# Performance work log

Measured on AMD Instinct MI355X. Metric: run time of the kernel, lower is better.

## Reference

```python
import jax, jax.numpy as jnp
import numpy as np

B, D, H, DH, NQ, NK = 64, 768, 8, 128, 256, 256


def _ln(x, g, b, eps=1e-5):
    m = x.mean(-1, keepdims=True)
    v = ((x - m) ** 2).mean(-1, keepdims=True)
    return (x - m) / jnp.sqrt(v + eps) * g + b


def setup_inputs() -> dict:
    key = jax.random.key(0)
    ks = jax.random.split(key, 16)
    w = lambda k, s: jax.random.normal(k, s, jnp.float32) * 0.02
    return {
        'emb_cause': jax.random.normal(ks[0], (B, D), jnp.float32),
        'emb_action': jax.random.normal(ks[1], (B, D), jnp.float32),
        'tok_cause': jax.random.normal(ks[2], (B, NK, D), jnp.float32),
        'tok_effect': jax.random.normal(ks[3], (B, NQ, D), jnp.float32),
        'fuse_ln_g': jnp.ones(2 * D), 'fuse_ln_b': jnp.zeros(2 * D),
        'fuse_w1': w(ks[4], (2 * D, D)), 'fuse_b1': jnp.zeros(D),
        'fuse_w2': w(ks[5], (D, D)), 'fuse_b2': jnp.zeros(D),
        'delta_ln_g': jnp.ones(D), 'delta_ln_b': jnp.zeros(D),
        'delta_w': w(ks[6], (D, D)), 'delta_b': jnp.zeros(D),
        'qg_w': w(ks[7], (D, H * DH)), 'qg_b': jnp.zeros(H * DH),
        'kg_w': w(ks[8], (D, H * DH)), 'kg_b': jnp.zeros(H * DH),
        'eff_ln_g': jnp.ones(D), 'eff_ln_b': jnp.zeros(D),
        'eff_w1': w(ks[9], (D, D)), 'eff_b1': jnp.zeros(D),
        'eff_w2': w(ks[10], (D, D)), 'eff_b2': jnp.zeros(D),
        'u_w': w(ks[11], (D, H * DH)),
        'v_w': w(ks[12], (D, H * DH)),
        'logit_scale': jnp.zeros(()),
    }


def reference(emb_cause, emb_action, tok_cause, tok_effect,
              fuse_ln_g, fuse_ln_b, fuse_w1, fuse_b1, fuse_w2, fuse_b2,
              delta_ln_g, delta_ln_b, delta_w, delta_b,
              qg_w, qg_b, kg_w, kg_b,
              eff_ln_g, eff_ln_b, eff_w1, eff_b1, eff_w2, eff_b2,
              u_w, v_w, logit_scale):
    # fuse: LN -> Linear -> GELU(exact) -> Linear (dropout = identity, eval)
    ctx_in = jnp.concatenate([emb_cause, emb_action], axis=-1)  # (B, 2D)
    h = jax.nn.gelu(_ln(ctx_in, fuse_ln_g, fuse_ln_b) @ fuse_w1 + fuse_b1, approximate=False)
    ctx = h @ fuse_w2 + fuse_b2  # (B, D)

    delta_e = _ln(ctx, delta_ln_g, delta_ln_b) @ delta_w + delta_b  # (B, D)
    pooled_effect = tok_effect.mean(axis=1)  # (B, D)
    e_shifted = pooled_effect + delta_e

    eh = jax.nn.gelu(_ln(ctx, eff_ln_g, eff_ln_b) @ eff_w1 + eff_b1, approximate=False)
    effect_pred = eh @ eff_w2 + eff_b2  # (B, D)

    q_gate = 1.0 + jnp.tanh(jax.nn.silu(ctx @ qg_w + qg_b)).reshape(B, H, DH)
    k_gate = 1.0 + jnp.tanh(jax.nn.silu(ctx @ kg_w + kg_b)).reshape(B, H, DH)

    # logit bias: torch code materializes (B,H,Nq,Nk,Dh); equivalent math is a
    # per-head inner product u.v (independent of q) broadcast over Nq.
    u = (e_shifted @ u_w).reshape(B, H, DH)            # (B, H, Dh)
    v = (tok_cause @ v_w).reshape(B, NK, H, DH)        # (B, Nk, H, Dh)
    bias = jnp.einsum('bhd,bkhd->bhk', u, v) / np.float32(np.sqrt(DH))
    logit_bias = jnp.exp(logit_scale) * jnp.broadcast_to(bias[:, :, None, :], (B, H, NQ, NK))

    return (q_gate, k_gate, e_shifted, delta_e, logit_bias, effect_pred)
```

## Files before the change

### kernel.cpp

```cpp
#include <hip/hip_runtime.h>
#include <math.h>

#define TPB 256

typedef float vf4 __attribute__((ext_vector_type(4)));

__device__ __forceinline__ float gelu_f(float x) {
    return 0.5f * x * (1.0f + erff(x * 0.70710678118654752f));
}
__device__ __forceinline__ float gate_f(float x) {
    float si = x / (1.0f + expf(-x));
    return 1.0f + tanhf(si);
}

template <class XL>
__device__ __forceinline__ void gemm_tile(XL xload, const float* __restrict__ W, int Wld, int cb,
                                          int k0, int kslice, float* part, int totN, int gcol, int s,
                                          float* __restrict__ xs, float* __restrict__ wt)
{
    const int t = threadIdx.x;
    const int tr4 = (t >> 4) << 2;
    const int tc4 = (t & 15) << 2;
    const int a  = t >> 5, kk = t & 31;
    const int wk = t >> 6, wc = t & 63;
    float xv[8], wv[8];
#pragma unroll
    for (int j = 0; j < 8; ++j) {
        xv[j] = xload(a + 8 * j, k0 + kk);
        wv[j] = W[(size_t)(k0 + wk + 4 * j) * Wld + cb + wc];
    }
    float acc[4][4] = {{0.f,0.f,0.f,0.f},{0.f,0.f,0.f,0.f},{0.f,0.f,0.f,0.f},{0.f,0.f,0.f,0.f}};
    for (int kc = 0; kc < kslice; kc += 32) {
#pragma unroll
        for (int j = 0; j < 8; ++j) {
            xs[kk * 68 + a + 8 * j] = xv[j];
            wt[(wk + 4 * j) * 68 + wc] = wv[j];
        }
        __syncthreads();
        int kn = kc + 32;
        if (kn < kslice) {
#pragma unroll
            for (int j = 0; j < 8; ++j) {
                xv[j] = xload(a + 8 * j, k0 + kn + kk);
                wv[j] = W[(size_t)(k0 + kn + wk + 4 * j) * Wld + cb + wc];
            }
        }
#pragma unroll
        for (int k = 0; k < 32; ++k) {
            float4 xq = *(const float4*)&xs[k * 68 + tr4];
            float4 wq = *(const float4*)&wt[k * 68 + tc4];
            acc[0][0] += xq.x * wq.x; acc[0][1] += xq.x * wq.y; acc[0][2] += xq.x * wq.z; acc[0][3] += xq.x * wq.w;
            acc[1][0] += xq.y * wq.x; acc[1][1] += xq.y * wq.y; acc[1][2] += xq.y * wq.z; acc[1][3] += xq.y * wq.w;
            acc[2][0] += xq.z * wq.x; acc[2][1] += xq.z * wq.y; acc[2][2] += xq.z * wq.z; acc[2][3] += xq.z * wq.w;
            acc[3][0] += xq.w * wq.x; acc[3][1] += xq.w * wq.y; acc[3][2] += xq.w * wq.z; acc[3][3] += xq.w * wq.w;
        }
        __syncthreads();
    }
    float* pp = part + (size_t)(s * 64 + tr4) * totN + gcol + tc4;
#pragma unroll
    for (int i = 0; i < 4; ++i)
#pragma unroll
        for (int j = 0; j < 4; ++j)
            pp[i * totN + j] = acc[i][j];
}

#define GEMM_LDS __shared__ float xs[32 * 68]; __shared__ float wt[32 * 68];

__device__ __forceinline__ void pool_task(const float* __restrict__ tok_effect,
                                          float* __restrict__ pp, int m, int t)
{
    int cch = m % 3, b = (m / 3) % 64, qz = m / 192;
    int c = cch * TPB + t;
    const float* base = tok_effect + (size_t)(b * 256 + qz * 64) * 768 + c;
    float s = 0.f;
#pragma unroll 16
    for (int q = 0; q < 64; ++q) s += __builtin_nontemporal_load(base + (size_t)q * 768);
    pp[(qz * 64 + b) * 768 + c] = s;
}

struct G1Args {
    const float *ec, *ea, *flg, *flb, *w1;
    const float *dg, *db, *eg, *eb, *delta_w, *eff_w1;
    const float *tok_effect;
    float *part1, *pp, *stats1, *gW1, *bW1, *dgW, *dbW, *egW, *ebW;
};
__global__ __launch_bounds__(256) void k_g1(G1Args A)
{
    GEMM_LDS;
    __shared__ float red[8];
    const int t = threadIdx.x;
    if (blockIdx.x < 144) {
        int ct = blockIdx.x % 12, s = blockIdx.x / 12;
        auto xl = [&](int r, int k) {
            float raw = (k < 768) ? A.ec[r * 768 + k] : A.ea[r * 768 + (k - 768)];
            return raw * A.flg[k];
        };
        gemm_tile(xl, A.w1, 768, ct * 64, s * 128, 128, A.part1, 768, ct * 64, s, xs, wt);
    } else if (blockIdx.x < 528) {
        pool_task(A.tok_effect, A.pp, blockIdx.x - 144, t);
    } else if (blockIdx.x < 592) {
        int r = blockIdx.x - 528;
        float sum = 0.f, sq = 0.f;
#pragma unroll
        for (int j = 0; j < 6; ++j) {
            int c = t + j * TPB;
            float x = (c < 768) ? A.ec[r * 768 + c] : A.ea[r * 768 + (c - 768)];
            sum += x; sq += x * x;
        }
#pragma unroll
        for (int o_ = 32; o_ > 0; o_ >>= 1) { sum += __shfl_xor(sum, o_); sq += __shfl_xor(sq, o_); }
        if ((t & 63) == 0) { red[t >> 6] = sum; red[4 + (t >> 6)] = sq; }
        __syncthreads();
        if (t == 0) {
            float s = red[0] + red[1] + red[2] + red[3];
            float q = red[4] + red[5] + red[6] + red[7];
            float mean = s * (1.f / 1536.f);
            A.stats1[2 * r]     = mean;
            A.stats1[2 * r + 1] = rsqrtf(q * (1.f / 1536.f) - mean * mean + 1e-5f);
        }
    } else {
        int m = blockIdx.x - 592;
        int id = m / 12, chunk = m % 12;
        const float* vec; const float* W; int K; float* out;
        switch (id) {
            case 0: vec = A.flg; W = A.w1;      K = 1536; out = A.gW1; break;
            case 1: vec = A.flb; W = A.w1;      K = 1536; out = A.bW1; break;
            case 2: vec = A.dg;  W = A.delta_w; K = 768;  out = A.dgW; break;
            case 3: vec = A.db;  W = A.delta_w; K = 768;  out = A.dbW; break;
            case 4: vec = A.eg;  W = A.eff_w1;  K = 768;  out = A.egW; break;
            default: vec = A.eb; W = A.eff_w1;  K = 768;  out = A.ebW; break;
        }
        int col = chunk * 64 + (t & 63);
        int stripe = t >> 6;
        float acc = 0.f;
#pragma unroll 16
        for (int c = stripe; c < K; c += 4)
            acc += vec[c] * W[(size_t)c * 768 + col];
        xs[stripe * 64 + (t & 63)] = acc;
        __syncthreads();
        if (t < 64)
            out[chunk * 64 + t] = xs[t] + xs[64 + t] + xs[128 + t] + xs[192 + t];
    }
}

struct G2Args {
    const float *part1, *b1, *w2, *stats1, *gW1, *bW1;
    const float *tok_effect;
    float *part2, *pp;
};
__global__ __launch_bounds__(256) void k_g2(G2Args A)
{
    GEMM_LDS;
    if (blockIdx.x >= 144) {
        pool_task(A.tok_effect, A.pp, blockIdx.x - 144 + 384, threadIdx.x);
        return;
    }
    int ct = blockIdx.x % 12, s = blockIdx.x / 12;
    auto xl = [&](int r, int k) {
        float v = 0.f;
#pragma unroll
        for (int q = 0; q < 12; ++q) v += A.part1[(size_t)(q * 64 + r) * 768 + k];
        float m = A.stats1[2 * r], rs = A.stats1[2 * r + 1];
        return gelu_f(rs * (v - m * A.gW1[k]) + A.bW1[k] + A.b1[k]);
    };
    gemm_tile(xl, A.w2, 768, ct * 64, s * 64, 64, A.part2, 768, ct * 64, s, xs, wt);
}

struct GAArgs {
    const float *part2, *b2, *dg, *eg;
    const float *delta_w, *eff_w1, *qg_w, *kg_w;
    float *partA, *stats2;
};
__global__ __launch_bounds__(256) void k_gA(GAArgs A)
{
    GEMM_LDS;
    __shared__ float red[8];
    const int t = threadIdx.x;
    if (blockIdx.x >= 448) {
        int r = blockIdx.x - 448;
        float sum = 0.f, sq = 0.f;
#pragma unroll
        for (int j = 0; j < 3; ++j) {
            int c = t + j * TPB;
            float x = A.b2[c];
#pragma unroll
            for (int q = 0; q < 12; ++q) x += A.part2[(size_t)(q * 64 + r) * 768 + c];
            sum += x; sq += x * x;
        }
#pragma unroll
        for (int o_ = 32; o_ > 0; o_ >>= 1) { sum += __shfl_xor(sum, o_); sq += __shfl_xor(sq, o_); }
        if ((t & 63) == 0) { red[t >> 6] = sum; red[4 + (t >> 6)] = sq; }
        __syncthreads();
        if (t == 0) {
            float s = red[0] + red[1] + red[2] + red[3];
            float q = red[4] + red[5] + red[6] + red[7];
            float mean = s * (1.f / 768.f);
            A.stats2[2 * r]     = mean;
            A.stats2[2 * r + 1] = rsqrtf(q * (1.f / 768.f) - mean * mean + 1e-5f);
        }
        return;
    }
    int ct = blockIdx.x % 56, s = blockIdx.x / 56;
    auto ctxv = [&](int r, int k) {
        float v = A.b2[k];
#pragma unroll
        for (int q = 0; q < 12; ++q) v += A.part2[(size_t)(q * 64 + r) * 768 + k];
        return v;
    };
    if (ct < 12) {
        auto xl = [&](int r, int k) { return ctxv(r, k) * A.dg[k]; };
        gemm_tile(xl, A.delta_w, 768, ct * 64, s * 96, 96, A.partA, 3584, ct * 64, s, xs, wt);
    } else if (ct < 24) {
        auto xl = [&](int r, int k) { return ctxv(r, k) * A.eg[k]; };
        gemm_tile(xl, A.eff_w1, 768, (ct - 12) * 64, s * 96, 96, A.partA, 3584, ct * 64, s, xs, wt);
    } else {
        auto xl = [&](int r, int k) { return ctxv(r, k); };
        const float* W = (ct < 40) ? A.qg_w : A.kg_w;
        int cb = (ct < 40) ? (ct - 24) * 64 : (ct - 40) * 64;
        gemm_tile(xl, W, 1024, cb, s * 96, 96, A.partA, 3584, ct * 64, s, xs, wt);
    }
}

struct MidArgs {
    const float *partA, *pp, *stats2, *dgW, *dbW, *egW, *ebW;
    const float *delta_b, *eff_b1, *qg_b, *kg_b, *eff_w2, *u_w;
    float *partB, *out_de, *out_es, *out_qg, *out_kg;
};
__global__ __launch_bounds__(256) void k_mid(MidArgs A)
{
    GEMM_LDS;
    const int t = threadIdx.x;
    if (blockIdx.x < 28) {
#pragma unroll
        for (int ii = 0; ii < 32; ++ii) {
            int idx = blockIdx.x * TPB + t + ii * 7168;
            int r = idx / 3584, c = idx - r * 3584;
            if (c >= 768 && c < 1536) continue;
            float v = 0.f;
#pragma unroll
            for (int q = 0; q < 8; ++q) v += A.partA[(size_t)(q * 64 + r) * 3584 + c];
            if (c < 768) {
                float m = A.stats2[2 * r], rs = A.stats2[2 * r + 1];
                float de = rs * (v - m * A.dgW[c]) + A.dbW[c] + A.delta_b[c];
                A.out_de[r * 768 + c] = de;
                float s4 = A.pp[r * 768 + c] + A.pp[(64 + r) * 768 + c]
                         + A.pp[(128 + r) * 768 + c] + A.pp[(192 + r) * 768 + c];
                A.out_es[r * 768 + c] = de + s4 * (1.f / 256.f);
            } else if (c < 2560) {
                A.out_qg[r * 1024 + (c - 1536)] = gate_f(v + A.qg_b[c - 1536]);
            } else {
                A.out_kg[r * 1024 + (c - 2560)] = gate_f(v + A.kg_b[c - 2560]);
            }
        }
    } else {
        int m = blockIdx.x - 28;
        int ct = m % 28, s = m / 28;
        if (ct < 12) {
            auto xl = [&](int r, int k) {
                float v = 0.f;
#pragma unroll
                for (int q = 0; q < 8; ++q) v += A.partA[(size_t)(q * 64 + r) * 3584 + 768 + k];
                float mm = A.stats2[2 * r], rs = A.stats2[2 * r + 1];
                return gelu_f(rs * (v - mm * A.egW[k]) + A.ebW[k] + A.eff_b1[k]);
            };
            gemm_tile(xl, A.eff_w2, 768, ct * 64, s * 96, 96, A.partB, 1792, ct * 64, s, xs, wt);
        } else {
            auto xl = [&](int r, int k) {
                float v = 0.f;
#pragma unroll
                for (int q = 0; q < 8; ++q) v += A.partA[(size_t)(q * 64 + r) * 3584 + k];
                float mm = A.stats2[2 * r], rs = A.stats2[2 * r + 1];
                float de = rs * (v - mm * A.dgW[k]) + A.dbW[k] + A.delta_b[k];
                float s4 = A.pp[r * 768 + k] + A.pp[(64 + r) * 768 + k]
                         + A.pp[(128 + r) * 768 + k] + A.pp[(192 + r) * 768 + k];
                return de + s4 * (1.f / 256.f);
            };
            gemm_tile(xl, A.u_w, 1024, (ct - 12) * 64, s * 96, 96, A.partB, 1792, ct * 64, s, xs, wt);
        }
    }
}

__global__ __launch_bounds__(256) void k_tail(const float* __restrict__ partB, const float* __restrict__ eff_b2,
                                              const float* __restrict__ v_w,
                                              float* __restrict__ out_ep, float* __restrict__ wu)
{
    const int t = threadIdx.x;
    if (blockIdx.x < 6) {
#pragma unroll
        for (int ii = 0; ii < 32; ++ii) {
            int idx = blockIdx.x * TPB + t + ii * 1536;
            int r = idx / 768, c = idx - r * 768;
            float v = eff_b2[c];
#pragma unroll
            for (int q = 0; q < 8; ++q) v += partB[(size_t)(q * 64 + r) * 1792 + c];
            out_ep[r * 768 + c] = v;
        }
    } else {
        __shared__ float us[64 * 132];
        int m = blockIdx.x - 6;
        int h = m / 12, ctile = m % 12;
        for (int n = t; n < 8192; n += TPB) {
            int b = n >> 7, d = n & 127;
            float v = 0.f;
#pragma unroll
            for (int q = 0; q < 8; ++q) v += partB[(size_t)(q * 64 + b) * 1792 + 768 + h * 128 + d];
            us[b * 132 + d] = v;
        }
        __syncthreads();
        int c = ctile * 64 + (t >> 2);
        int bo = t & 3;
        const float* vr = v_w + (size_t)c * 1024 + h * 128;
        float acc[16];
#pragma unroll
        for (int i = 0; i < 16; ++i) acc[i] = 0.f;
        for (int d = 0; d < 128; d += 4) {
            float4 w4 = *(const float4*)(vr + d);
#pragma unroll
            for (int i = 0; i < 16; ++i) {
                const float* ub = &us[(4 * i + bo) * 132 + d];
                acc[i] += w4.x * ub[0] + w4.y * ub[1] + w4.z * ub[2] + w4.w * ub[3];
            }
        }
#pragma unroll
        for (int i = 0; i < 16; ++i) {
            int b = 4 * i + bo;
            wu[(b * 8 + h) * 768 + c] = acc[i];
        }
    }
}

__global__ __launch_bounds__(512) void k_biasbc(const float* __restrict__ tok_cause, const float* __restrict__ wu,
                         const float* __restrict__ ls_ptr, float* __restrict__ out_lb)
{
    int b = blockIdx.x, kt = blockIdx.y;
    __shared__ float wuh[8 * 768];
    __shared__ float bsm[8 * 32];
    for (int n = threadIdx.x; n < 6144; n += 512)
        wuh[n] = wu[b * 6144 + n];
    __syncthreads();
    const int lane = threadIdx.x & 63, w = threadIdx.x >> 6;
    vf4 wur[3][8];
#pragma unroll
    for (int j = 0; j < 3; ++j)
#pragma unroll
        for (int h = 0; h < 8; ++h)
            wur[j][h] = *(const vf4*)&wuh[h * 768 + (lane + 64 * j) * 4];
    float scale = expf(ls_ptr[0]) * 0.08838834764831845f;
#pragma unroll
    for (int rr = 0; rr < 4; ++rr) {
        int rl = w * 4 + rr;
        int row = kt * 32 + rl;
        const vf4* tr = (const vf4*)(tok_cause + ((size_t)b * 256 + row) * 768);
        vf4 t0 = tr[lane];
        vf4 t1 = tr[lane + 64];
        vf4 t2 = tr[lane + 128];
        float acc[8];
#pragma unroll
        for (int h = 0; h < 8; ++h) {
            acc[h] = t0.x * wur[0][h].x + t0.y * wur[0][h].y + t0.z * wur[0][h].z + t0.w * wur[0][h].w
                   + t1.x * wur[1][h].x + t1.y * wur[1][h].y + t1.z * wur[1][h].z + t1.w * wur[1][h].w
                   + t2.x * wur[2][h].x + t2.y * wur[2][h].y + t2.z * wur[2][h].z + t2.w * wur[2][h].w;
        }
#pragma unroll
        for (int h = 0; h < 8; ++h) {
            float vv = acc[h];
#pragma unroll
            for (int o_ = 32; o_ > 0; o_ >>= 1) vv += __shfl_xor(vv, o_);
            if (lane == 0) bsm[h * 32 + rl] = vv * scale;
        }
    }
    __syncthreads();
    const vf4* bs4 = (const vf4*)bsm;
    vf4* o4 = (vf4*)out_lb;
    int v = threadIdx.x & 7, sq0 = threadIdx.x >> 3;
#pragma unroll
    for (int it = 0; it < 32; ++it) {
        int seg = sq0 + it * 64;
        int h = seg >> 8, q = seg & 255;
        vf4 val = bs4[h * 8 + v];
        __builtin_nontemporal_store(val, &o4[(((size_t)(b * 8 + h) * 256 + q) << 6) + kt * 8 + v]);
    }
}

extern "C" void kernel_launch(void* const* d_in, const int* in_sizes, int n_in,
                              void* d_out, int out_size, void* d_ws, size_t ws_size,
                              hipStream_t stream)
{
    (void)in_sizes; (void)n_in; (void)out_size; (void)ws_size;
    const float* emb_cause  = (const float*)d_in[0];
    const float* emb_action = (const float*)d_in[1];
    const float* tok_cause  = (const float*)d_in[2];
    const float* tok_effect = (const float*)d_in[3];
    const float* fuse_ln_g  = (const float*)d_in[4];
    const float* fuse_ln_b  = (const float*)d_in[5];
    const float* fuse_w1    = (const float*)d_in[6];
    const float* fuse_b1    = (const float*)d_in[7];
    const float* fuse_w2    = (const float*)d_in[8];
    const float* fuse_b2    = (const float*)d_in[9];
    const float* delta_ln_g = (const float*)d_in[10];
    const float* delta_ln_b = (const float*)d_in[11];
    const float* delta_w    = (const float*)d_in[12];
    const float* delta_b    = (const float*)d_in[13];
    const float* qg_w       = (const float*)d_in[14];
    const float* qg_b       = (const float*)d_in[15];
    const float* kg_w       = (const float*)d_in[16];
    const float* kg_b       = (const float*)d_in[17];
    const float* eff_ln_g   = (const float*)d_in[18];
    const float* eff_ln_b   = (const float*)d_in[19];
    const float* eff_w1     = (const float*)d_in[20];
    const float* eff_b1     = (const float*)d_in[21];
    const float* eff_w2     = (const float*)d_in[22];
    const float* eff_b2     = (const float*)d_in[23];
    const float* u_w        = (const float*)d_in[24];
    const float* v_w        = (const float*)d_in[25];
    const float* logit_sc   = (const float*)d_in[26];

    float* ws = (float*)d_ws;
    float* pp     = ws + 0;
    float* wu     = ws + 196608;
    float* stats1 = ws + 589824;
    float* stats2 = ws + 589952;
    float* gW1    = ws + 590080;
    float* bW1    = ws + 590848;
    float* dgW    = ws + 591616;
    float* dbW    = ws + 592384;
    float* egW    = ws + 593152;
    float* ebW    = ws + 593920;

    float* out    = (float*)d_out;
    float* out_qg = out + 0;
    float* out_kg = out + 65536;
    float* out_es = out + 131072;
    float* out_de = out + 180224;
    float* out_lb = out + 229376;
    float* out_ep = out + 33783808;

    float* pbase = out_lb + 20000000;
    float* part1 = pbase;
    float* part2 = pbase + 589824;
    float* partA = pbase + 1179648;
    float* partB = pbase + 3014656;

    {
        G1Args A; A.ec = emb_cause; A.ea = emb_action;
        A.flg = fuse_ln_g; A.flb = fuse_ln_b; A.w1 = fuse_w1;
        A.dg = delta_ln_g; A.db = delta_ln_b; A.eg = eff_ln_g; A.eb = eff_ln_b;
        A.delta_w = delta_w; A.eff_w1 = eff_w1;
        A.tok_effect = tok_effect;
        A.part1 = part1; A.pp = pp; A.stats1 = stats1;
        A.gW1 = gW1; A.bW1 = bW1; A.dgW = dgW; A.dbW = dbW; A.egW = egW; A.ebW = ebW;
        k_g1<<<664, TPB, 0, stream>>>(A);
    }
    {
        G2Args A; A.part1 = part1; A.b1 = fuse_b1; A.w2 = fuse_w2;
        A.stats1 = stats1; A.gW1 = gW1; A.bW1 = bW1;
        A.tok_effect = tok_effect; A.part2 = part2; A.pp = pp;
        k_g2<<<528, TPB, 0, stream>>>(A);
    }
    {
        GAArgs A; A.part2 = part2; A.b2 = fuse_b2;
        A.dg = delta_ln_g; A.eg = eff_ln_g;
        A.delta_w = delta_w; A.eff_w1 = eff_w1; A.qg_w = qg_w; A.kg_w = kg_w;
        A.partA = partA; A.stats2 = stats2;
        k_gA<<<512, TPB, 0, stream>>>(A);
    }
    {
        MidArgs M; M.partA = partA; M.pp = pp; M.stats2 = stats2;
        M.dgW = dgW; M.dbW = dbW; M.egW = egW; M.ebW = ebW;
        M.delta_b = delta_b; M.eff_b1 = eff_b1; M.qg_b = qg_b; M.kg_b = kg_b;
        M.eff_w2 = eff_w2; M.u_w = u_w; M.partB = partB;
        M.out_de = out_de; M.out_es = out_es; M.out_qg = out_qg; M.out_kg = out_kg;
        k_mid<<<252, TPB, 0, stream>>>(M);
    }
    k_tail<<<102, TPB, 0, stream>>>(partB, eff_b2, v_w, out_ep, wu);
    k_biasbc<<<dim3(64, 8), 512, 0, stream>>>(tok_cause, wu, logit_sc, out_lb);
}
```

Measured before the change: 142.7 us.

## Fuse k_tail and k_biasbc into one kernel recomputing v_w·u per block

Merges the effect-pred reduction, the v_w·u projection and the bias broadcast into a single launch. Each bias block now sums partB and computes its own wu slice (8x768) in shared memory, so the intermediate wu buffer and one kernel launch go away. Blocks now cover 64 key rows instead of 32, which halves the grid for the bias part. In exchange, the v_w product (about 3 MB of weights) is recomputed by each of the 256 blocks, which is four times per batch row and adds redundant L2 traffic and FLOPs. partB also moves from the output scratch area into the workspace.

```diff
diff --git a/kernel.cpp b/kernel.cpp
--- a/kernel.cpp
+++ b/kernel.cpp
@@ -280,65 +280,52 @@
     }
 }
 
-__global__ __launch_bounds__(256) void k_tail(const float* __restrict__ partB, const float* __restrict__ eff_b2,
-                                              const float* __restrict__ v_w,
-                                              float* __restrict__ out_ep, float* __restrict__ wu)
+__global__ __launch_bounds__(512) void k_biaswu(const float* __restrict__ partB, const float* __restrict__ v_w,
+                          const float* __restrict__ tok_cause, const float* __restrict__ ls_ptr,
+                          const float* __restrict__ eff_b2,
+                          float* __restrict__ out_ep, float* __restrict__ out_lb)
 {
     const int t = threadIdx.x;
-    if (blockIdx.x < 6) {
-#pragma unroll
-        for (int ii = 0; ii < 32; ++ii) {
-            int idx = blockIdx.x * TPB + t + ii * 1536;
+    if (blockIdx.x >= 256) {
+        int blk = blockIdx.x - 256;
+#pragma unroll
+        for (int ii = 0; ii < 16; ++ii) {
+            int idx = blk * 512 + t + ii * 3072;
             int r = idx / 768, c = idx - r * 768;
             float v = eff_b2[c];
 #pragma unroll
             for (int q = 0; q < 8; ++q) v += partB[(size_t)(q * 64 + r) * 1792 + c];
             out_ep[r * 768 + c] = v;
         }
-    } else {
-        __shared__ float us[64 * 132];
-        int m = blockIdx.x - 6;
-        int h = m / 12, ctile = m % 12;
-        for (int n = t; n < 8192; n += TPB) {
-            int b = n >> 7, d = n & 127;
-            float v = 0.f;
-#pragma unroll
-            for (int q = 0; q < 8; ++q) v += partB[(size_t)(q * 64 + b) * 1792 + 768 + h * 128 + d];
-            us[b * 132 + d] = v;
-        }
-        __syncthreads();
-        int c = ctile * 64 + (t >> 2);
-        int bo = t & 3;
-        const float* vr = v_w + (size_t)c * 1024 + h * 128;
-        float acc[16];
-#pragma unroll
-        for (int i = 0; i < 16; ++i) acc[i] = 0.f;
-        for (int d = 0; d < 128; d += 4) {
-            float4 w4 = *(const float4*)(vr + d);
-#pragma unroll
-            for (int i = 0; i < 16; ++i) {
-                const float* ub = &us[(4 * i + bo) * 132 + d];
-                acc[i] += w4.x * ub[0] + w4.y * ub[1] + w4.z * ub[2] + w4.w * ub[3];
-            }
-        }
-#pragma unroll
-        for (int i = 0; i < 16; ++i) {
-            int b = 4 * i + bo;
-            wu[(b * 8 + h) * 768 + c] = acc[i];
-        }
-    }
-}
-
-__global__ __launch_bounds__(512) void k_biasbc(const float* __restrict__ tok_cause, const float* __restrict__ wu,
-                         const float* __restrict__ ls_ptr, float* __restrict__ out_lb)
-{
-    int b = blockIdx.x, kt = blockIdx.y;
-    __shared__ float wuh[8 * 768];
-    __shared__ float bsm[8 * 32];
-    for (int n = threadIdx.x; n < 6144; n += 512)
-        wuh[n] = wu[b * 6144 + n];
+        return;
+    }
+    int b = blockIdx.x >> 2, kt4 = blockIdx.x & 3;
+    __shared__ float us[1024];
+    __shared__ float wuh[6144];
+    __shared__ float bsm[8 * 64];
+    for (int e = t; e < 1024; e += 512) {
+        float v = 0.f;
+#pragma unroll
+        for (int q = 0; q < 8; ++q) v += partB[(size_t)(q * 64 + b) * 1792 + 768 + e];
+        us[e] = v;
+    }
     __syncthreads();
-    const int lane = threadIdx.x & 63, w = threadIdx.x >> 6;
+#pragma unroll
+    for (int j = 0; j < 12; ++j) {
+        int idx = j * 512 + t;
+        int h = idx / 768, c = idx - h * 768;
+        const vf4* vr = (const vf4*)(v_w + (size_t)c * 1024 + h * 128);
+        const vf4* ur = (const vf4*)(us + h * 128);
+        float acc = 0.f;
+#pragma unroll
+        for (int d4 = 0; d4 < 32; ++d4) {
+            vf4 w4 = vr[d4], u4 = ur[d4];
+            acc += w4.x * u4.x + w4.y * u4.y + w4.z * u4.z + w4.w * u4.w;
+        }
+        wuh[h * 768 + c] = acc;
+    }
+    __syncthreads();
+    const int lane = t & 63, w = t >> 6;
     vf4 wur[3][8];
 #pragma unroll
     for (int j = 0; j < 3; ++j)
@@ -347,9 +334,9 @@
             wur[j][h] = *(const vf4*)&wuh[h * 768 + (lane + 64 * j) * 4];
     float scale = expf(ls_ptr[0]) * 0.08838834764831845f;
 #pragma unroll
-    for (int rr = 0; rr < 4; ++rr) {
-        int rl = w * 4 + rr;
-        int row = kt * 32 + rl;
+    for (int rr = 0; rr < 8; ++rr) {
+        int rl = w * 8 + rr;
+        int row = kt4 * 64 + rl;
         const vf4* tr = (const vf4*)(tok_cause + ((size_t)b * 256 + row) * 768);
         vf4 t0 = tr[lane];
         vf4 t1 = tr[lane + 64];
@@ -366,19 +353,19 @@
             float vv = acc[h];
 #pragma unroll
             for (int o_ = 32; o_ > 0; o_ >>= 1) vv += __shfl_xor(vv, o_);
-            if (lane == 0) bsm[h * 32 + rl] = vv * scale;
+            if (lane == 0) bsm[h * 64 + rl] = vv * scale;
         }
     }
     __syncthreads();
     const vf4* bs4 = (const vf4*)bsm;
     vf4* o4 = (vf4*)out_lb;
-    int v = threadIdx.x & 7, sq0 = threadIdx.x >> 3;
-#pragma unroll
-    for (int it = 0; it < 32; ++it) {
-        int seg = sq0 + it * 64;
+    int v = t & 15, sq0 = t >> 4;
+#pragma unroll
+    for (int it = 0; it < 64; ++it) {
+        int seg = sq0 + it * 32;
         int h = seg >> 8, q = seg & 255;
-        vf4 val = bs4[h * 8 + v];
-        __builtin_nontemporal_store(val, &o4[(((size_t)(b * 8 + h) * 256 + q) << 6) + kt * 8 + v]);
+        vf4 val = bs4[h * 16 + v];
+        __builtin_nontemporal_store(val, &o4[(((size_t)(b * 8 + h) * 256 + q) << 6) + kt4 * 16 + v]);
     }
 }
 
@@ -417,15 +404,15 @@
 
     float* ws = (float*)d_ws;
     float* pp     = ws + 0;
-    float* wu     = ws + 196608;
-    float* stats1 = ws + 589824;
-    float* stats2 = ws + 589952;
-    float* gW1    = ws + 590080;
-    float* bW1    = ws + 590848;
-    float* dgW    = ws + 591616;
-    float* dbW    = ws + 592384;
-    float* egW    = ws + 593152;
-    float* ebW    = ws + 593920;
+    float* partB  = ws + 196608;
+    float* stats1 = ws + 1114112;
+    float* stats2 = ws + 1114240;
+    float* gW1    = ws + 1114368;
+    float* bW1    = ws + 1115136;
+    float* dgW    = ws + 1115904;
+    float* dbW    = ws + 1116672;
+    float* egW    = ws + 1117440;
+    float* ebW    = ws + 1118208;
 
     float* out    = (float*)d_out;
     float* out_qg = out + 0;
@@ -439,7 +426,6 @@
     float* part1 = pbase;
     float* part2 = pbase + 589824;
     float* partA = pbase + 1179648;
-    float* partB = pbase + 3014656;
 
     {
         G1Args A; A.ec = emb_cause; A.ea = emb_action;
@@ -472,6 +458,5 @@
         M.out_de = out_de; M.out_es = out_es; M.out_qg = out_qg; M.out_kg = out_kg;
         k_mid<<<252, TPB, 0, stream>>>(M);
     }
-    k_tail<<<102, TPB, 0, stream>>>(partB, eff_b2, v_w, out_ep, wu);
-    k_biasbc<<<dim3(64, 8), 512, 0, stream>>>(tok_cause, wu, logit_sc, out_lb);
-}
+    k_biaswu<<<262, 512, 0, stream>>>(partB, v_w, tok_cause, logit_sc, eff_b2, out_ep, out_lb);
+}
```

Measured after the change: 211.6 us. 1.48x slower.
